# Performance work log

Measured on AMD Instinct MI355X. Metric: run time of the kernel, lower is better.

## Reference

```python
import jax, jax.numpy as jnp
import numpy as np
from jax import lax

B, N, E, H = 512, 128, 256, 8
D = E // H
CLIP = 10.0
NEG = -1e9  # finite stand-in for -inf (backward-safe, math-identical after softmax)


def setup_inputs() -> dict:
    key = jax.random.key(0)
    ks = jax.random.split(key, 5)
    s = lambda k, shape: jax.random.normal(k, shape, jnp.float32) * 0.05
    return {
        "node_embeddings": jax.random.normal(ks[0], (B, N, E), jnp.float32),
        "Wqkv": s(ks[1], (E, 3 * E)), "bqkv": jnp.zeros((3 * E,), jnp.float32),
        "Wfix": s(ks[2], (E, E)), "bfix": jnp.zeros((E,), jnp.float32),
        "Wstep": s(ks[3], (2 * E, E)), "bstep": jnp.zeros((E,), jnp.float32),
        "Wmlp": s(ks[4], (E, E)), "bmlp": jnp.zeros((E,), jnp.float32),
    }


def reference(node_embeddings, Wqkv, bqkv, Wfix, bfix, Wstep, bstep, Wmlp, bmlp):
    scale = 1.0 / np.sqrt(D)
    graph_emb = node_embeddings.mean(axis=1)                       # (B,E)
    qkv = node_embeddings @ Wqkv + bqkv                            # (B,N,3E)
    k, v, logit_k = jnp.split(qkv, 3, axis=-1)
    kh = k.reshape(B, N, H, D).transpose(0, 2, 1, 3)               # (B,H,N,D)
    vh = v.reshape(B, N, H, D).transpose(0, 2, 1, 3)               # (B,H,N,D)
    fixed = graph_emb @ Wfix + bfix                                # (B,E)
    first = node_embeddings[:, 0, :]                               # (B,E)
    bidx = jnp.arange(B)

    def step(carry, _):
        current, visited, logp_sum = carry
        last = node_embeddings[bidx, current]                      # gather last action emb (B,E)
        q = fixed + (jnp.concatenate([first, last], axis=-1) @ Wstep + bstep)
        qh = q.reshape(B, H, D)                                    # single query per head
        attn = jnp.einsum('bhd,bhnd->bhn', qh, kh) * scale
        attn = jnp.where(visited[:, None, :], NEG, attn)
        attn = jax.nn.softmax(attn, axis=-1)
        ctx = jnp.einsum('bhn,bhnd->bhd', attn, vh).reshape(B, E)
        x = ctx @ Wmlp + bmlp                                      # (B,E)
        logits = jnp.einsum('be,bne->bn', x, logit_k) * scale      # (B,N)
        logits = jnp.tanh(logits) * CLIP
        logits = jnp.where(visited, NEG, logits)
        log_p = jax.nn.log_softmax(logits, axis=-1)
        action = jnp.argmax(log_p, axis=-1)                        # greedy decode
        chosen = jnp.take_along_axis(log_p, action[:, None], axis=1)[:, 0]
        visited = visited | jax.nn.one_hot(action, N, dtype=bool)
        return (action, visited, logp_sum + chosen), action

    visited0 = jnp.zeros((B, N), bool).at[:, 0].set(True)
    current0 = jnp.zeros((B,), jnp.int32)
    (_, _, logp_sum), seq = lax.scan(
        step, (current0, visited0, jnp.zeros((B,), jnp.float32)), None, length=N - 1)
    return logp_sum                                                # (B,) summed log-prob of tour
```

## Files before the change

kernel.cpp:

```cpp
#include <hip/hip_runtime.h>
#include <math.h>


#define B_ 512
#define N_ 128
#define E_ 256
#define H_ 8
#define D_ 32
#define NEG (-1.0e9f)
#define CLIPV 10.0f
#define SCALE 0.17677669529663688110f

typedef float v2f __attribute__((ext_vector_type(2)));

__device__ __forceinline__ void pkfma(v2f& acc, v2f a, v2f b) {
  asm("v_pk_fma_f32 %0, %1, %2, %0" : "+v"(acc) : "v"(a), "v"(b));
}

template <int CTRL>
__device__ __forceinline__ float dpp_f(float x) {
  int r = __builtin_amdgcn_update_dpp(__float_as_int(x), __float_as_int(x),
                                      CTRL, 0xf, 0xf, false);
  return __int_as_float(r);
}
template <int CTRL, int RM>
__device__ __forceinline__ float dpp_mv(float x, float idv) {
  int r = __builtin_amdgcn_update_dpp(__float_as_int(idv), __float_as_int(x),
                                      CTRL, RM, 0xf, false);
  return __int_as_float(r);
}
__device__ __forceinline__ float wred_max(float v) {
  v = fmaxf(v, dpp_f<0xB1>(v));
  v = fmaxf(v, dpp_f<0x4E>(v));
  v = fmaxf(v, dpp_f<0x124>(v));
  v = fmaxf(v, dpp_f<0x128>(v));
  v = fmaxf(v, dpp_mv<0x142, 0xa>(v, -1e38f));
  v = fmaxf(v, dpp_mv<0x143, 0xc>(v, -1e38f));
  return __int_as_float(__builtin_amdgcn_readlane(__float_as_int(v), 63));
}
__device__ __forceinline__ float wred_sum(float v) {
  v += dpp_f<0xB1>(v);
  v += dpp_f<0x4E>(v);
  v += dpp_f<0x124>(v);
  v += dpp_f<0x128>(v);
  v += dpp_mv<0x142, 0xa>(v, 0.0f);
  v += dpp_mv<0x143, 0xc>(v, 0.0f);
  return __int_as_float(__builtin_amdgcn_readlane(__float_as_int(v), 63));
}

__global__ void k0_prep(const float* __restrict__ Wqkv, const float* __restrict__ bqkv,
                        const float* __restrict__ Wmlp, const float* __restrict__ bmlp,
                        float* __restrict__ Wc, float* __restrict__ bc,
                        float* __restrict__ wc2, float* __restrict__ cconst) {
  int t = threadIdx.x;
  int blk = blockIdx.x;
  __shared__ float row_s[E_];
  if (blk < E_) {
    int g = blk;
    row_s[t] = Wqkv[g * 768 + 512 + t];
    __syncthreads();
    int f = t;
    const float4* wm4 = (const float4*)(Wmlp + f * E_);
    const float4* w34 = (const float4*)row_s;
    float acc = 0.f;
#pragma unroll 8
    for (int j = 0; j < E_ / 4; ++j) {
      float4 a = w34[j]; float4 bv = wm4[j];
      acc += a.x * bv.x + a.y * bv.y + a.z * bv.z + a.w * bv.w;
    }
    Wc[g * E_ + f] = acc;
  } else {
    int f = t;
    float a1 = 0.f, a2 = 0.f;
    for (int e = 0; e < E_; ++e) {
      a1 += bqkv[512 + e] * Wmlp[f * E_ + e];
      a2 += Wqkv[f * 768 + 512 + e] * bmlp[e];
    }
    bc[f] = a1;
    wc2[f] = a2;
    if (t == 0) {
      float c = 0.f;
      for (int e = 0; e < E_; ++e) c += bqkv[512 + e] * bmlp[e];
      *cconst = c;
    }
  }
}

__global__ __launch_bounds__(256, 2)
void k_gemm(const float* __restrict__ emb, const float* __restrict__ Wqkv,
            const float* __restrict__ bqkv,
            const float* __restrict__ Wc, const float* __restrict__ bc,
            const float* __restrict__ Wstep, const float* __restrict__ qbase,
            float* __restrict__ kk_, float* __restrict__ vv_,
            float* __restrict__ lk2, float* __restrict__ qtab,
            int ncc, int tmask) {
  __shared__ float As[256 * 64];
  int t = threadIdx.x;
  int r0 = blockIdx.x * 64;
  {
    int m = t >> 2;
    int c0 = t & 3;
    const float4* e4 = (const float4*)emb;
#pragma unroll
    for (int p = 0; p < 16; ++p) {
      int c4 = c0 + p * 4;
      float4 a = e4[(size_t)(r0 + m) * 64 + c4];
      As[(c4 * 4 + 0) * 64 + m] = a.x;
      As[(c4 * 4 + 1) * 64 + m] = a.y;
      As[(c4 * 4 + 2) * 64 + m] = a.z;
      As[(c4 * 4 + 3) * 64 + m] = a.w;
    }
  }
  __syncthreads();
  int tx = t & 15, ty = t >> 4;
  const float4* As4 = (const float4*)As;
  for (int cc = 0; cc < ncc; ++cc) {
    const float* Bp; int ldb4; const float* bias; float* outp;
    int colbase = (cc & 1) * 128;
    switch (cc >> 1) {
      case 0:  Bp = Wqkv + colbase;          ldb4 = 192; bias = bqkv + colbase;       outp = kk_; break;
      case 1:  Bp = Wqkv + 256 + colbase;    ldb4 = 192; bias = bqkv + 256 + colbase; outp = vv_; break;
      case 2:  Bp = Wc + colbase;            ldb4 = 64;  bias = bc + colbase;         outp = lk2; break;
      default: Bp = Wstep + 65536 + colbase; ldb4 = 64;
               bias = qbase + (size_t)(r0 >> 7) * 256 + colbase;                      outp = qtab; break;
    }
    const float4* B4 = (const float4*)Bp;
    float acc[4][8];
#pragma unroll
    for (int i = 0; i < 4; ++i)
#pragma unroll
      for (int j = 0; j < 8; ++j) acc[i][j] = 0.f;

#pragma unroll 4
    for (int kk = 0; kk < 256; ++kk) {
      float4 b0 = B4[kk * ldb4 + tx * 2];
      float4 b1 = B4[kk * ldb4 + tx * 2 + 1];
      float4 av = As4[kk * 16 + ty];
      float a_[4] = {av.x, av.y, av.z, av.w};
#pragma unroll
      for (int i = 0; i < 4; ++i) {
        acc[i][0] += a_[i] * b0.x; acc[i][1] += a_[i] * b0.y;
        acc[i][2] += a_[i] * b0.z; acc[i][3] += a_[i] * b0.w;
        acc[i][4] += a_[i] * b1.x; acc[i][5] += a_[i] * b1.y;
        acc[i][6] += a_[i] * b1.z; acc[i][7] += a_[i] * b1.w;
      }
    }
    float bj[8];
#pragma unroll
    for (int j = 0; j < 8; ++j) bj[j] = bias ? bias[tx * 8 + j] : 0.f;
    int tr = (tmask >> (cc >> 1)) & 1;
    if (!tr) {
#pragma unroll
      for (int i = 0; i < 4; ++i) {
        int row = r0 + ty * 4 + i;
        float4 o0 = make_float4(acc[i][0] + bj[0], acc[i][1] + bj[1], acc[i][2] + bj[2], acc[i][3] + bj[3]);
        float4 o1 = make_float4(acc[i][4] + bj[4], acc[i][5] + bj[5], acc[i][6] + bj[6], acc[i][7] + bj[7]);
        float4* o4 = (float4*)(outp + (size_t)row * 256 + colbase + tx * 8);
        o4[0] = o0; o4[1] = o1;
      }
    } else {
#pragma unroll
      for (int i = 0; i < 4; ++i) {
        int row = r0 + ty * 4 + i;
        int bb = row >> 7, nn = row & 127;
        float* op = outp + (size_t)bb * 32768 + nn;
#pragma unroll
        for (int j = 0; j < 8; ++j)
          op[(size_t)(colbase + tx * 8 + j) * 128] = acc[i][j] + bj[j];
      }
    }
  }
}

__global__ void k_qbase(const float* __restrict__ emb, const float* __restrict__ Wfix,
                        const float* __restrict__ bfix, const float* __restrict__ Wstep,
                        const float* __restrict__ bstep, float* __restrict__ qbase) {
  int b = blockIdx.x, t = threadIdx.x;
  __shared__ float ge[E_], fi[E_];
  const float* eb = emb + (size_t)b * N_ * E_;
  float s = 0.f;
#pragma unroll 8
  for (int n = 0; n < N_; ++n) s += eb[n * E_ + t];
  ge[t] = s * (1.0f / 128.0f);
  fi[t] = eb[t];
  __syncthreads();
  float acc = bfix[t] + bstep[t];
#pragma unroll 4
  for (int g = 0; g < E_; ++g)
    acc += ge[g] * Wfix[g * E_ + t] + fi[g] * Wstep[g * E_ + t];
  qbase[b * E_ + t] = acc;
}

__global__ void k_c(const float* __restrict__ emb, const float* __restrict__ wc2,
                    const float* __restrict__ cconst, float* __restrict__ cvec) {
  __shared__ float w[E_];
  int t = threadIdx.x;
  w[t] = wc2[t];
  __syncthreads();
  int row = blockIdx.x * 256 + t;
  const float4* e4 = (const float4*)(emb + (size_t)row * E_);
  const float4* w4 = (const float4*)w;
  float acc = 0.f;
#pragma unroll 8
  for (int j = 0; j < E_ / 4; ++j) {
    float4 a = e4[j], bv = w4[j];
    acc += a.x * bv.x + a.y * bv.y + a.z * bv.z + a.w * bv.w;
  }
  cvec[row] = acc + *cconst;
}

__global__ __attribute__((amdgpu_flat_work_group_size(512, 512), amdgpu_waves_per_eu(2, 2)))
void k_roll(const float* __restrict__ emb, const float* __restrict__ Wstep,
            const float* __restrict__ kT, const float* __restrict__ vv_,
            const float* __restrict__ lkT,
            const float* __restrict__ qbase, const float* __restrict__ cvec,
            const float* __restrict__ qtab, int use_qtab,
            float* __restrict__ out) {
  int lt = threadIdx.x;
  int b = blockIdx.x;
  int h = lt >> 6;
  int j = lt & 63;

  __shared__ float sq_lds[128 * 260];
  __shared__ float work[6144];
  float* at_s  = work;
  float* ctx_s = work + 1024;
  float* zp    = work + 1280;

  if (use_qtab) {
    const float4* qt4 = (const float4*)(qtab + (size_t)b * 32768);
#pragma unroll
    for (int p = 0; p < 16; ++p) {
      int idx = p * 512 + lt;
      int n = idx >> 6, c4 = idx & 63;
      float4 a = qt4[idx];
      *(float4*)(sq_lds + n * 260 + c4 * 4) = a;
    }
  } else {
    float* At = work;
    float* Bs = work + 2048;
    const float4* eb4 = (const float4*)(emb + (size_t)b * 32768);
    const float* W2 = Wstep + 65536;
    int n0 = (lt & 31) * 4;
    int e0 = (lt >> 5) * 16;
    float acc[4][16];
#pragma unroll
    for (int i = 0; i < 4; ++i)
#pragma unroll
      for (int jj = 0; jj < 16; ++jj) acc[i][jj] = 0.f;

    for (int gc = 0; gc < 16; ++gc) {
      {
        int n = lt & 127, q4g = lt >> 7;
        float4 a = eb4[n * 64 + gc * 4 + q4g];
        At[(q4g * 4 + 0) * 128 + n] = a.x;
        At[(q4g * 4 + 1) * 128 + n] = a.y;
        At[(q4g * 4 + 2) * 128 + n] = a.z;
        At[(q4g * 4 + 3) * 128 + n] = a.w;
      }
      {
        const float4* w4 = (const float4*)(W2 + gc * 16 * 256);
        ((float4*)Bs)[lt] = w4[lt];
        ((float4*)Bs)[lt + 512] = w4[lt + 512];
      }
      __syncthreads();
#pragma unroll
      for (int gi = 0; gi < 16; ++gi) {
        float4 a4 = *(const float4*)(At + gi * 128 + n0);
        const float4* bp = (const float4*)(Bs + gi * 256 + e0);
        float4 b0 = bp[0], b1 = bp[1], b2 = bp[2], b3 = bp[3];
        float av[4] = {a4.x, a4.y, a4.z, a4.w};
        float bv[16] = {b0.x, b0.y, b0.z, b0.w, b1.x, b1.y, b1.z, b1.w,
                        b2.x, b2.y, b2.z, b2.w, b3.x, b3.y, b3.z, b3.w};
#pragma unroll
        for (int i = 0; i < 4; ++i)
#pragma unroll
          for (int jj = 0; jj < 16; ++jj) acc[i][jj] += av[i] * bv[jj];
      }
      __syncthreads();
    }
    const float* qb = qbase + (size_t)b * 256;
    float qbr[16];
#pragma unroll
    for (int jj = 0; jj < 16; ++jj) qbr[jj] = qb[e0 + jj];
#pragma unroll
    for (int i = 0; i < 4; ++i)
#pragma unroll
      for (int jj = 0; jj < 16; ++jj)
        sq_lds[(n0 + i) * 260 + e0 + jj] = acc[i][jj] + qbr[jj];
  }
  __syncthreads();
  __builtin_amdgcn_sched_barrier(0);

  const float* kTb = kT + (size_t)b * 32768;
  const float* vb  = vv_ + (size_t)b * 32768;
  const float* lTb = lkT + (size_t)b * 32768;

  v2f k0p[16], k1p[16];
#pragma unroll
  for (int d = 0; d < 16; ++d) {
    k0p[d] = (v2f){kTb[(h * 32 + 2 * d) * 128 + j],      kTb[(h * 32 + 2 * d + 1) * 128 + j]};
    k1p[d] = (v2f){kTb[(h * 32 + 2 * d) * 128 + j + 64], kTb[(h * 32 + 2 * d + 1) * 128 + j + 64]};
    asm("" : "+v"(k0p[d]));
    asm("" : "+v"(k1p[d]));
  }
  int e_own = h * 32 + (j & 31), nh = j >> 5;
  v2f vp[32];
#pragma unroll
  for (int m = 0; m < 32; ++m) {
    vp[m] = (v2f){vb[(nh * 64 + 2 * m) * 256 + e_own], vb[(nh * 64 + 2 * m + 1) * 256 + e_own]};
    asm("" : "+v"(vp[m]));
  }
  v2f l0p[16], l1p[16];
#pragma unroll
  for (int e = 0; e < 16; ++e) {
    l0p[e] = (v2f){lTb[(h * 32 + 2 * e) * 128 + j],      lTb[(h * 32 + 2 * e + 1) * 128 + j]};
    l1p[e] = (v2f){lTb[(h * 32 + 2 * e) * 128 + j + 64], lTb[(h * 32 + 2 * e + 1) * 128 + j + 64]};
    asm("" : "+v"(l0p[e]));
    asm("" : "+v"(l1p[e]));
  }
  float cv_lo = cvec[b * 128 + j];
  float cv_hi = cvec[b * 128 + j + 64];
  int vis_lo = (j == 0) ? 1 : 0, vis_hi = 0;
  int cur = 0;
  float lp = 0.f;
  int rof0 = j * 12;
  int rof1 = rof0 + 768;
  int csw  = h ^ ((j >> 2) & 7);

#pragma unroll 1
  for (int it = 0; it < N_ - 1; ++it) {
    const float4* q4 = (const float4*)(sq_lds + cur * 260 + h * 32);
    v2f s00 = {0.f, 0.f}, s01 = {0.f, 0.f}, s10 = {0.f, 0.f}, s11 = {0.f, 0.f};
#pragma unroll
    for (int dd = 0; dd < 8; ++dd) {
      float4 qv = q4[dd];
      v2f qa = {qv.x, qv.y}, qb = {qv.z, qv.w};
      pkfma(s00, qa, k0p[2 * dd]);
      pkfma(s01, qb, k0p[2 * dd + 1]);
      pkfma(s10, qa, k1p[2 * dd]);
      pkfma(s11, qb, k1p[2 * dd + 1]);
    }
    float slo = vis_lo ? NEG : ((s00.x + s00.y) + (s01.x + s01.y)) * SCALE;
    float shi = vis_hi ? NEG : ((s10.x + s10.y) + (s11.x + s11.y)) * SCALE;
    float m = wred_max(fmaxf(slo, shi));
    float elo = expf(slo - m), ehi = expf(shi - m);
    at_s[h * 128 + j] = elo;
    at_s[h * 128 + 64 + j] = ehi;
    float inv = 1.0f / wred_sum(elo + ehi);
    const float4* a4 = (const float4*)(at_s + h * 128 + nh * 64);
    v2f c0 = {0.f, 0.f}, c1 = {0.f, 0.f};
#pragma unroll
    for (int mm = 0; mm < 16; ++mm) {
      float4 av = a4[mm];
      v2f aa = {av.x, av.y}, ab = {av.z, av.w};
      pkfma(c0, aa, vp[2 * mm]);
      pkfma(c1, ab, vp[2 * mm + 1]);
    }
    float c = (c0.x + c0.y) + (c1.x + c1.y);
    c += __shfl_xor(c, 32);
    c *= inv;
    if (j < 32) ctx_s[h * 32 + j] = c;
    const float4* cx4 = (const float4*)(ctx_s + h * 32);
    v2f z00 = {0.f, 0.f}, z01 = {0.f, 0.f}, z10 = {0.f, 0.f}, z11 = {0.f, 0.f};
#pragma unroll
    for (int ee = 0; ee < 8; ++ee) {
      float4 cv = cx4[ee];
      v2f ca = {cv.x, cv.y}, cb = {cv.z, cv.w};
      pkfma(z00, ca, l0p[2 * ee]);
      pkfma(z01, cb, l0p[2 * ee + 1]);
      pkfma(z10, ca, l1p[2 * ee]);
      pkfma(z11, cb, l1p[2 * ee + 1]);
    }
    float* zpw = zp + (it & 1) * 1536;
    zpw[rof0 + csw] = (z00.x + z00.y) + (z01.x + z01.y);
    zpw[rof1 + csw] = (z10.x + z10.y) + (z11.x + z11.y);
    __syncthreads();

    const float4* zr0 = (const float4*)(zpw + rof0);
    const float4* zr1 = (const float4*)(zpw + rof1);
    float4 za = zr0[0], zb = zr0[1], zc = zr1[0], zd = zr1[1];
    float zlo = cv_lo + ((za.x + za.y) + (za.z + za.w)) + ((zb.x + zb.y) + (zb.z + zb.w));
    float zhi = cv_hi + ((zc.x + zc.y) + (zc.z + zc.w)) + ((zd.x + zd.y) + (zd.z + zd.w));
    float zmlo = vis_lo ? -1e30f : zlo;
    float zmhi = vis_hi ? -1e30f : zhi;
    float vmax = wred_max(fmaxf(zmlo, zmhi));
    unsigned long long blo = __ballot(zmlo == vmax);
    int action;
    if (blo) action = __ffsll((unsigned long long)blo) - 1;
    else     action = 63 + __ffsll((unsigned long long)__ballot(zmhi == vmax));
    if (h == 0) {
      float lmax = CLIPV * tanhf(vmax * SCALE);
      float tlo = vis_lo ? 0.f : expf(CLIPV * tanhf(zlo * SCALE) - 10.0f);
      float thi = vis_hi ? 0.f : expf(CLIPV * tanhf(zhi * SCALE) - 10.0f);
      float S = wred_sum(tlo + thi);
      lp += lmax - 10.0f - logf(S);
    }
    cur = action;
    vis_lo |= (action == j);
    vis_hi |= (action == j + 64);
  }
  if (lt == 0) out[b] = lp;
}

extern "C" void kernel_launch(void* const* d_in, const int* in_sizes, int n_in,
                              void* d_out, int out_size, void* d_ws, size_t ws_size,
                              hipStream_t stream) {
  (void)in_sizes; (void)n_in; (void)out_size;
  const float* emb   = (const float*)d_in[0];
  const float* Wqkv  = (const float*)d_in[1];
  const float* bqkv  = (const float*)d_in[2];
  const float* Wfix  = (const float*)d_in[3];
  const float* bfix  = (const float*)d_in[4];
  const float* Wstep = (const float*)d_in[5];
  const float* bstep = (const float*)d_in[6];
  const float* Wmlp  = (const float*)d_in[7];
  const float* bmlp  = (const float*)d_in[8];
  float* out = (float*)d_out;
  float* ws = (float*)d_ws;

  const size_t NBE = (size_t)B_ * N_ * E_;
  float* kk_    = ws;
  float* vv_    = ws + NBE;
  float* lk2    = ws + 2 * NBE;
  float* qbase  = ws + 3 * NBE;
  float* cvec   = qbase + 131072;
  float* Wc     = cvec + 65536;
  float* bc     = Wc + 65536;
  float* wc2    = bc + 256;
  float* cconst = wc2 + 256;
  size_t qoff   = 3 * NBE + 262720;
  float* qtab   = ws + qoff;
  int use_qtab  = (ws_size >= (qoff + NBE) * sizeof(float)) ? 1 : 0;

  hipLaunchKernelGGL(k0_prep, dim3(257), dim3(256), 0, stream,
                     Wqkv, bqkv, Wmlp, bmlp, Wc, bc, wc2, cconst);
  hipLaunchKernelGGL(k_qbase, dim3(512), dim3(256), 0, stream,
                     emb, Wfix, bfix, Wstep, bstep, qbase);
  hipLaunchKernelGGL(k_c, dim3(256), dim3(256), 0, stream,
                     emb, wc2, cconst, cvec);
  hipLaunchKernelGGL(k_gemm, dim3(1024), dim3(256), 0, stream,
                     emb, Wqkv, bqkv, Wc, bc, Wstep, qbase,
                     kk_, vv_, lk2, qtab, use_qtab ? 8 : 6, 0b0101);
  hipLaunchKernelGGL(k_roll, dim3(512), dim3(512), 0, stream,
                     emb, Wstep, kk_, vv_, lk2, qbase, cvec, qtab, use_qtab, out);
}
```

Before: 1.165 ms.

## Split rollout kernel; read query table from global instead of staging in LDS

Adds a specialized rollout kernel for the precomputed query-table path that drops the 133KB LDS query staging and instead reads the per-step query row straight from global memory using a wave-uniform index. The LDS footprint shrinks to about 17KB and the launch bounds no longer pin waves-per-EU, which could allow more blocks per CU and removes the upfront table copy. The cost is a global/L2 load on the serial per-step critical path, where an LDS read was used before. The fallback kernel keeps the original behaviour.

```diff
diff --git a/kernel.cpp b/kernel.cpp
--- a/kernel.cpp
+++ b/kernel.cpp
@@ -209,88 +209,19 @@
   cvec[row] = acc + *cconst;
 }
 
-__global__ __attribute__((amdgpu_flat_work_group_size(512, 512), amdgpu_waves_per_eu(2, 2)))
-void k_roll(const float* __restrict__ emb, const float* __restrict__ Wstep,
-            const float* __restrict__ kT, const float* __restrict__ vv_,
-            const float* __restrict__ lkT,
-            const float* __restrict__ qbase, const float* __restrict__ cvec,
-            const float* __restrict__ qtab, int use_qtab,
-            float* __restrict__ out) {
+__global__ __launch_bounds__(512)
+void k_rollq(const float* __restrict__ kT, const float* __restrict__ vv_,
+             const float* __restrict__ lkT, const float* __restrict__ cvec,
+             const float* __restrict__ qtab, float* __restrict__ out) {
   int lt = threadIdx.x;
   int b = blockIdx.x;
   int h = lt >> 6;
   int j = lt & 63;
 
-  __shared__ float sq_lds[128 * 260];
-  __shared__ float work[6144];
+  __shared__ float work[4352];
   float* at_s  = work;
   float* ctx_s = work + 1024;
   float* zp    = work + 1280;
-
-  if (use_qtab) {
-    const float4* qt4 = (const float4*)(qtab + (size_t)b * 32768);
-#pragma unroll
-    for (int p = 0; p < 16; ++p) {
-      int idx = p * 512 + lt;
-      int n = idx >> 6, c4 = idx & 63;
-      float4 a = qt4[idx];
-      *(float4*)(sq_lds + n * 260 + c4 * 4) = a;
-    }
-  } else {
-    float* At = work;
-    float* Bs = work + 2048;
-    const float4* eb4 = (const float4*)(emb + (size_t)b * 32768);
-    const float* W2 = Wstep + 65536;
-    int n0 = (lt & 31) * 4;
-    int e0 = (lt >> 5) * 16;
-    float acc[4][16];
-#pragma unroll
-    for (int i = 0; i < 4; ++i)
-#pragma unroll
-      for (int jj = 0; jj < 16; ++jj) acc[i][jj] = 0.f;
-
-    for (int gc = 0; gc < 16; ++gc) {
-      {
-        int n = lt & 127, q4g = lt >> 7;
-        float4 a = eb4[n * 64 + gc * 4 + q4g];
-        At[(q4g * 4 + 0) * 128 + n] = a.x;
-        At[(q4g * 4 + 1) * 128 + n] = a.y;
-        At[(q4g * 4 + 2) * 128 + n] = a.z;
-        At[(q4g * 4 + 3) * 128 + n] = a.w;
-      }
-      {
-        const float4* w4 = (const float4*)(W2 + gc * 16 * 256);
-        ((float4*)Bs)[lt] = w4[lt];
-        ((float4*)Bs)[lt + 512] = w4[lt + 512];
-      }
-      __syncthreads();
-#pragma unroll
-      for (int gi = 0; gi < 16; ++gi) {
-        float4 a4 = *(const float4*)(At + gi * 128 + n0);
-        const float4* bp = (const float4*)(Bs + gi * 256 + e0);
-        float4 b0 = bp[0], b1 = bp[1], b2 = bp[2], b3 = bp[3];
-        float av[4] = {a4.x, a4.y, a4.z, a4.w};
-        float bv[16] = {b0.x, b0.y, b0.z, b0.w, b1.x, b1.y, b1.z, b1.w,
-                        b2.x, b2.y, b2.z, b2.w, b3.x, b3.y, b3.z, b3.w};
-#pragma unroll
-        for (int i = 0; i < 4; ++i)
-#pragma unroll
-          for (int jj = 0; jj < 16; ++jj) acc[i][jj] += av[i] * bv[jj];
-      }
-      __syncthreads();
-    }
-    const float* qb = qbase + (size_t)b * 256;
-    float qbr[16];
-#pragma unroll
-    for (int jj = 0; jj < 16; ++jj) qbr[jj] = qb[e0 + jj];
-#pragma unroll
-    for (int i = 0; i < 4; ++i)
-#pragma unroll
-      for (int jj = 0; jj < 16; ++jj)
-        sq_lds[(n0 + i) * 260 + e0 + jj] = acc[i][jj] + qbr[jj];
-  }
-  __syncthreads();
-  __builtin_amdgcn_sched_barrier(0);
 
   const float* kTb = kT + (size_t)b * 32768;
   const float* vb  = vv_ + (size_t)b * 32768;
@@ -327,10 +258,12 @@
   int rof0 = j * 12;
   int rof1 = rof0 + 768;
   int csw  = h ^ ((j >> 2) & 7);
+  const float* qhb = qtab + ((size_t)b << 15) + (h << 5);
 
 #pragma unroll 1
   for (int it = 0; it < N_ - 1; ++it) {
-    const float4* q4 = (const float4*)(sq_lds + cur * 260 + h * 32);
+    int curu = __builtin_amdgcn_readfirstlane(cur);
+    const float4* q4 = (const float4*)(qhb + (curu << 8));
     v2f s00 = {0.f, 0.f}, s01 = {0.f, 0.f}, s10 = {0.f, 0.f}, s11 = {0.f, 0.f};
 #pragma unroll
     for (int dd = 0; dd < 8; ++dd) {
@@ -403,6 +336,190 @@
   if (lt == 0) out[b] = lp;
 }
 
+__global__ __attribute__((amdgpu_flat_work_group_size(512, 512), amdgpu_waves_per_eu(2, 2)))
+void k_roll(const float* __restrict__ emb, const float* __restrict__ Wstep,
+            const float* __restrict__ kT, const float* __restrict__ vv_,
+            const float* __restrict__ lkT,
+            const float* __restrict__ qbase, const float* __restrict__ cvec,
+            float* __restrict__ out) {
+  int lt = threadIdx.x;
+  int b = blockIdx.x;
+  int h = lt >> 6;
+  int j = lt & 63;
+
+  __shared__ float sq_lds[128 * 260];
+  __shared__ float work[6144];
+  float* at_s  = work;
+  float* ctx_s = work + 1024;
+  float* zp    = work + 1280;
+
+  {
+    float* At = work;
+    float* Bs = work + 2048;
+    const float4* eb4 = (const float4*)(emb + (size_t)b * 32768);
+    const float* W2 = Wstep + 65536;
+    int n0 = (lt & 31) * 4;
+    int e0 = (lt >> 5) * 16;
+    float acc[4][16];
+#pragma unroll
+    for (int i = 0; i < 4; ++i)
+#pragma unroll
+      for (int jj = 0; jj < 16; ++jj) acc[i][jj] = 0.f;
+
+    for (int gc = 0; gc < 16; ++gc) {
+      {
+        int n = lt & 127, q4g = lt >> 7;
+        float4 a = eb4[n * 64 + gc * 4 + q4g];
+        At[(q4g * 4 + 0) * 128 + n] = a.x;
+        At[(q4g * 4 + 1) * 128 + n] = a.y;
+        At[(q4g * 4 + 2) * 128 + n] = a.z;
+        At[(q4g * 4 + 3) * 128 + n] = a.w;
+      }
+      {
+        const float4* w4 = (const float4*)(W2 + gc * 16 * 256);
+        ((float4*)Bs)[lt] = w4[lt];
+        ((float4*)Bs)[lt + 512] = w4[lt + 512];
+      }
+      __syncthreads();
+#pragma unroll
+      for (int gi = 0; gi < 16; ++gi) {
+        float4 a4 = *(const float4*)(At + gi * 128 + n0);
+        const float4* bp = (const float4*)(Bs + gi * 256 + e0);
+        float4 b0 = bp[0], b1 = bp[1], b2 = bp[2], b3 = bp[3];
+        float av[4] = {a4.x, a4.y, a4.z, a4.w};
+        float bv[16] = {b0.x, b0.y, b0.z, b0.w, b1.x, b1.y, b1.z, b1.w,
+                        b2.x, b2.y, b2.z, b2.w, b3.x, b3.y, b3.z, b3.w};
+#pragma unroll
+        for (int i = 0; i < 4; ++i)
+#pragma unroll
+          for (int jj = 0; jj < 16; ++jj) acc[i][jj] += av[i] * bv[jj];
+      }
+      __syncthreads();
+    }
+    const float* qb = qbase + (size_t)b * 256;
+    float qbr[16];
+#pragma unroll
+    for (int jj = 0; jj < 16; ++jj) qbr[jj] = qb[e0 + jj];
+#pragma unroll
+    for (int i = 0; i < 4; ++i)
+#pragma unroll
+      for (int jj = 0; jj < 16; ++jj)
+        sq_lds[(n0 + i) * 260 + e0 + jj] = acc[i][jj] + qbr[jj];
+  }
+  __syncthreads();
+  __builtin_amdgcn_sched_barrier(0);
+
+  const float* kTb = kT + (size_t)b * 32768;
+  const float* vb  = vv_ + (size_t)b * 32768;
+  const float* lTb = lkT + (size_t)b * 32768;
+
+  v2f k0p[16], k1p[16];
+#pragma unroll
+  for (int d = 0; d < 16; ++d) {
+    k0p[d] = (v2f){kTb[(h * 32 + 2 * d) * 128 + j],      kTb[(h * 32 + 2 * d + 1) * 128 + j]};
+    k1p[d] = (v2f){kTb[(h * 32 + 2 * d) * 128 + j + 64], kTb[(h * 32 + 2 * d + 1) * 128 + j + 64]};
+    asm("" : "+v"(k0p[d]));
+    asm("" : "+v"(k1p[d]));
+  }
+  int e_own = h * 32 + (j & 31), nh = j >> 5;
+  v2f vp[32];
+#pragma unroll
+  for (int m = 0; m < 32; ++m) {
+    vp[m] = (v2f){vb[(nh * 64 + 2 * m) * 256 + e_own], vb[(nh * 64 + 2 * m + 1) * 256 + e_own]};
+    asm("" : "+v"(vp[m]));
+  }
+  v2f l0p[16], l1p[16];
+#pragma unroll
+  for (int e = 0; e < 16; ++e) {
+    l0p[e] = (v2f){lTb[(h * 32 + 2 * e) * 128 + j],      lTb[(h * 32 + 2 * e + 1) * 128 + j]};
+    l1p[e] = (v2f){lTb[(h * 32 + 2 * e) * 128 + j + 64], lTb[(h * 32 + 2 * e + 1) * 128 + j + 64]};
+    asm("" : "+v"(l0p[e]));
+    asm("" : "+v"(l1p[e]));
+  }
+  float cv_lo = cvec[b * 128 + j];
+  float cv_hi = cvec[b * 128 + j + 64];
+  int vis_lo = (j == 0) ? 1 : 0, vis_hi = 0;
+  int cur = 0;
+  float lp = 0.f;
+  int rof0 = j * 12;
+  int rof1 = rof0 + 768;
+  int csw  = h ^ ((j >> 2) & 7);
+
+#pragma unroll 1
+  for (int it = 0; it < N_ - 1; ++it) {
+    const float4* q4 = (const float4*)(sq_lds + cur * 260 + h * 32);
+    v2f s00 = {0.f, 0.f}, s01 = {0.f, 0.f}, s10 = {0.f, 0.f}, s11 = {0.f, 0.f};
+#pragma unroll
+    for (int dd = 0; dd < 8; ++dd) {
+      float4 qv = q4[dd];
+      v2f qa = {qv.x, qv.y}, qb = {qv.z, qv.w};
+      pkfma(s00, qa, k0p[2 * dd]);
+      pkfma(s01, qb, k0p[2 * dd + 1]);
+      pkfma(s10, qa, k1p[2 * dd]);
+      pkfma(s11, qb, k1p[2 * dd + 1]);
+    }
+    float slo = vis_lo ? NEG : ((s00.x + s00.y) + (s01.x + s01.y)) * SCALE;
+    float shi = vis_hi ? NEG : ((s10.x + s10.y) + (s11.x + s11.y)) * SCALE;
+    float m = wred_max(fmaxf(slo, shi));
+    float elo = expf(slo - m), ehi = expf(shi - m);
+    at_s[h * 128 + j] = elo;
+    at_s[h * 128 + 64 + j] = ehi;
+    float inv = 1.0f / wred_sum(elo + ehi);
+    const float4* a4 = (const float4*)(at_s + h * 128 + nh * 64);
+    v2f c0 = {0.f, 0.f}, c1 = {0.f, 0.f};
+#pragma unroll
+    for (int mm = 0; mm < 16; ++mm) {
+      float4 av = a4[mm];
+      v2f aa = {av.x, av.y}, ab = {av.z, av.w};
+      pkfma(c0, aa, vp[2 * mm]);
+      pkfma(c1, ab, vp[2 * mm + 1]);
+    }
+    float c = (c0.x + c0.y) + (c1.x + c1.y);
+    c += __shfl_xor(c, 32);
+    c *= inv;
+    if (j < 32) ctx_s[h * 32 + j] = c;
+    const float4* cx4 = (const float4*)(ctx_s + h * 32);
+    v2f z00 = {0.f, 0.f}, z01 = {0.f, 0.f}, z10 = {0.f, 0.f}, z11 = {0.f, 0.f};
+#pragma unroll
+    for (int ee = 0; ee < 8; ++ee) {
+      float4 cv = cx4[ee];
+      v2f ca = {cv.x, cv.y}, cb = {cv.z, cv.w};
+      pkfma(z00, ca, l0p[2 * ee]);
+      pkfma(z01, cb, l0p[2 * ee + 1]);
+      pkfma(z10, ca, l1p[2 * ee]);
+      pkfma(z11, cb, l1p[2 * ee + 1]);
+    }
+    float* zpw = zp + (it & 1) * 1536;
+    zpw[rof0 + csw] = (z00.x + z00.y) + (z01.x + z01.y);
+    zpw[rof1 + csw] = (z10.x + z10.y) + (z11.x + z11.y);
+    __syncthreads();
+
+    const float4* zr0 = (const float4*)(zpw + rof0);
+    const float4* zr1 = (const float4*)(zpw + rof1);
+    float4 za = zr0[0], zb = zr0[1], zc = zr1[0], zd = zr1[1];
+    float zlo = cv_lo + ((za.x + za.y) + (za.z + za.w)) + ((zb.x + zb.y) + (zb.z + zb.w));
+    float zhi = cv_hi + ((zc.x + zc.y) + (zc.z + zc.w)) + ((zd.x + zd.y) + (zd.z + zd.w));
+    float zmlo = vis_lo ? -1e30f : zlo;
+    float zmhi = vis_hi ? -1e30f : zhi;
+    float vmax = wred_max(fmaxf(zmlo, zmhi));
+    unsigned long long blo = __ballot(zmlo == vmax);
+    int action;
+    if (blo) action = __ffsll((unsigned long long)blo) - 1;
+    else     action = 63 + __ffsll((unsigned long long)__ballot(zmhi == vmax));
+    if (h == 0) {
+      float lmax = CLIPV * tanhf(vmax * SCALE);
+      float tlo = vis_lo ? 0.f : expf(CLIPV * tanhf(zlo * SCALE) - 10.0f);
+      float thi = vis_hi ? 0.f : expf(CLIPV * tanhf(zhi * SCALE) - 10.0f);
+      float S = wred_sum(tlo + thi);
+      lp += lmax - 10.0f - logf(S);
+    }
+    cur = action;
+    vis_lo |= (action == j);
+    vis_hi |= (action == j + 64);
+  }
+  if (lt == 0) out[b] = lp;
+}
+
 extern "C" void kernel_launch(void* const* d_in, const int* in_sizes, int n_in,
                               void* d_out, int out_size, void* d_ws, size_t ws_size,
                               hipStream_t stream) {
@@ -442,6 +559,11 @@
   hipLaunchKernelGGL(k_gemm, dim3(1024), dim3(256), 0, stream,
                      emb, Wqkv, bqkv, Wc, bc, Wstep, qbase,
                      kk_, vv_, lk2, qtab, use_qtab ? 8 : 6, 0b0101);
-  hipLaunchKernelGGL(k_roll, dim3(512), dim3(512), 0, stream,
-                     emb, Wstep, kk_, vv_, lk2, qbase, cvec, qtab, use_qtab, out);
-}
+  if (use_qtab) {
+    hipLaunchKernelGGL(k_rollq, dim3(512), dim3(512), 0, stream,
+                       kk_, vv_, lk2, cvec, qtab, out);
+  } else {
+    hipLaunchKernelGGL(k_roll, dim3(512), dim3(512), 0, stream,
+                       emb, Wstep, kk_, vv_, lk2, qbase, cvec, out);
+  }
+}
```

Result: no change. 1.176 ms (+1.0%).

## Move per-node query table to a global buffer and read it from memory per step

Applied to the files above, without the earlier changes.

The precomputed query table now always lives in a static device-global buffer filled by the GEMM kernel, so the fallback in-kernel GEMM path and workspace-size check are gone. The rollout kernel no longer stages the 128x256 table in LDS and instead loads the current node's query row directly from global memory each step using a uniform address. This cuts LDS use (about 133 KB down to about 17 KB per block), which should allow more blocks per CU and removes the upfront staging copy. In exchange, each step's query load goes to global memory (L2) instead of LDS, which lengthens the serial dependency chain.

```diff
diff --git a/kernel.cpp b/kernel.cpp
--- a/kernel.cpp
+++ b/kernel.cpp
@@ -10,6 +10,8 @@
 #define NEG (-1.0e9f)
 #define CLIPV 10.0f
 #define SCALE 0.17677669529663688110f
+
+__device__ float g_qtab[(size_t)B_ * N_ * E_];
 
 typedef float v2f __attribute__((ext_vector_type(2)));
 
@@ -92,8 +94,7 @@
             const float* __restrict__ Wc, const float* __restrict__ bc,
             const float* __restrict__ Wstep, const float* __restrict__ qbase,
             float* __restrict__ kk_, float* __restrict__ vv_,
-            float* __restrict__ lk2, float* __restrict__ qtab,
-            int ncc, int tmask) {
+            float* __restrict__ lk2, int ncc, int tmask) {
   __shared__ float As[256 * 64];
   int t = threadIdx.x;
   int r0 = blockIdx.x * 64;
@@ -122,7 +123,7 @@
       case 1:  Bp = Wqkv + 256 + colbase;    ldb4 = 192; bias = bqkv + 256 + colbase; outp = vv_; break;
       case 2:  Bp = Wc + colbase;            ldb4 = 64;  bias = bc + colbase;         outp = lk2; break;
       default: Bp = Wstep + 65536 + colbase; ldb4 = 64;
-               bias = qbase + (size_t)(r0 >> 7) * 256 + colbase;                      outp = qtab; break;
+               bias = qbase + (size_t)(r0 >> 7) * 256 + colbase;                      outp = g_qtab; break;
     }
     const float4* B4 = (const float4*)Bp;
     float acc[4][8];
@@ -209,88 +210,19 @@
   cvec[row] = acc + *cconst;
 }
 
-__global__ __attribute__((amdgpu_flat_work_group_size(512, 512), amdgpu_waves_per_eu(2, 2)))
-void k_roll(const float* __restrict__ emb, const float* __restrict__ Wstep,
-            const float* __restrict__ kT, const float* __restrict__ vv_,
-            const float* __restrict__ lkT,
-            const float* __restrict__ qbase, const float* __restrict__ cvec,
-            const float* __restrict__ qtab, int use_qtab,
-            float* __restrict__ out) {
+__global__ __launch_bounds__(512)
+void k_rollq(const float* __restrict__ kT, const float* __restrict__ vv_,
+             const float* __restrict__ lkT, const float* __restrict__ cvec,
+             float* __restrict__ out) {
   int lt = threadIdx.x;
   int b = blockIdx.x;
   int h = lt >> 6;
   int j = lt & 63;
 
-  __shared__ float sq_lds[128 * 260];
-  __shared__ float work[6144];
+  __shared__ float work[4352];
   float* at_s  = work;
   float* ctx_s = work + 1024;
   float* zp    = work + 1280;
-
-  if (use_qtab) {
-    const float4* qt4 = (const float4*)(qtab + (size_t)b * 32768);
-#pragma unroll
-    for (int p = 0; p < 16; ++p) {
-      int idx = p * 512 + lt;
-      int n = idx >> 6, c4 = idx & 63;
-      float4 a = qt4[idx];
-      *(float4*)(sq_lds + n * 260 + c4 * 4) = a;
-    }
-  } else {
-    float* At = work;
-    float* Bs = work + 2048;
-    const float4* eb4 = (const float4*)(emb + (size_t)b * 32768);
-    const float* W2 = Wstep + 65536;
-    int n0 = (lt & 31) * 4;
-    int e0 = (lt >> 5) * 16;
-    float acc[4][16];
-#pragma unroll
-    for (int i = 0; i < 4; ++i)
-#pragma unroll
-      for (int jj = 0; jj < 16; ++jj) acc[i][jj] = 0.f;
-
-    for (int gc = 0; gc < 16; ++gc) {
-      {
-        int n = lt & 127, q4g = lt >> 7;
-        float4 a = eb4[n * 64 + gc * 4 + q4g];
-        At[(q4g * 4 + 0) * 128 + n] = a.x;
-        At[(q4g * 4 + 1) * 128 + n] = a.y;
-        At[(q4g * 4 + 2) * 128 + n] = a.z;
-        At[(q4g * 4 + 3) * 128 + n] = a.w;
-      }
-      {
-        const float4* w4 = (const float4*)(W2 + gc * 16 * 256);
-        ((float4*)Bs)[lt] = w4[lt];
-        ((float4*)Bs)[lt + 512] = w4[lt + 512];
-      }
-      __syncthreads();
-#pragma unroll
-      for (int gi = 0; gi < 16; ++gi) {
-        float4 a4 = *(const float4*)(At + gi * 128 + n0);
-        const float4* bp = (const float4*)(Bs + gi * 256 + e0);
-        float4 b0 = bp[0], b1 = bp[1], b2 = bp[2], b3 = bp[3];
-        float av[4] = {a4.x, a4.y, a4.z, a4.w};
-        float bv[16] = {b0.x, b0.y, b0.z, b0.w, b1.x, b1.y, b1.z, b1.w,
-                        b2.x, b2.y, b2.z, b2.w, b3.x, b3.y, b3.z, b3.w};
-#pragma unroll
-        for (int i = 0; i < 4; ++i)
-#pragma unroll
-          for (int jj = 0; jj < 16; ++jj) acc[i][jj] += av[i] * bv[jj];
-      }
-      __syncthreads();
-    }
-    const float* qb = qbase + (size_t)b * 256;
-    float qbr[16];
-#pragma unroll
-    for (int jj = 0; jj < 16; ++jj) qbr[jj] = qb[e0 + jj];
-#pragma unroll
-    for (int i = 0; i < 4; ++i)
-#pragma unroll
-      for (int jj = 0; jj < 16; ++jj)
-        sq_lds[(n0 + i) * 260 + e0 + jj] = acc[i][jj] + qbr[jj];
-  }
-  __syncthreads();
-  __builtin_amdgcn_sched_barrier(0);
 
   const float* kTb = kT + (size_t)b * 32768;
   const float* vb  = vv_ + (size_t)b * 32768;
@@ -327,10 +259,12 @@
   int rof0 = j * 12;
   int rof1 = rof0 + 768;
   int csw  = h ^ ((j >> 2) & 7);
+  const float* qhb = g_qtab + ((size_t)b << 15) + (h << 5);
 
 #pragma unroll 1
   for (int it = 0; it < N_ - 1; ++it) {
-    const float4* q4 = (const float4*)(sq_lds + cur * 260 + h * 32);
+    int curu = __builtin_amdgcn_readfirstlane(cur);
+    const float4* q4 = (const float4*)(qhb + (curu << 8));
     v2f s00 = {0.f, 0.f}, s01 = {0.f, 0.f}, s10 = {0.f, 0.f}, s11 = {0.f, 0.f};
 #pragma unroll
     for (int dd = 0; dd < 8; ++dd) {
@@ -406,7 +340,7 @@
 extern "C" void kernel_launch(void* const* d_in, const int* in_sizes, int n_in,
                               void* d_out, int out_size, void* d_ws, size_t ws_size,
                               hipStream_t stream) {
-  (void)in_sizes; (void)n_in; (void)out_size;
+  (void)in_sizes; (void)n_in; (void)out_size; (void)ws_size;
   const float* emb   = (const float*)d_in[0];
   const float* Wqkv  = (const float*)d_in[1];
   const float* bqkv  = (const float*)d_in[2];
@@ -429,9 +363,6 @@
   float* bc     = Wc + 65536;
   float* wc2    = bc + 256;
   float* cconst = wc2 + 256;
-  size_t qoff   = 3 * NBE + 262720;
-  float* qtab   = ws + qoff;
-  int use_qtab  = (ws_size >= (qoff + NBE) * sizeof(float)) ? 1 : 0;
 
   hipLaunchKernelGGL(k0_prep, dim3(257), dim3(256), 0, stream,
                      Wqkv, bqkv, Wmlp, bmlp, Wc, bc, wc2, cconst);
@@ -441,7 +372,7 @@
                      emb, wc2, cconst, cvec);
   hipLaunchKernelGGL(k_gemm, dim3(1024), dim3(256), 0, stream,
                      emb, Wqkv, bqkv, Wc, bc, Wstep, qbase,
-                     kk_, vv_, lk2, qtab, use_qtab ? 8 : 6, 0b0101);
-  hipLaunchKernelGGL(k_roll, dim3(512), dim3(512), 0, stream,
-                     emb, Wstep, kk_, vv_, lk2, qbase, cvec, qtab, use_qtab, out);
-}
+                     kk_, vv_, lk2, 8, 0b0101);
+  hipLaunchKernelGGL(k_rollq, dim3(512), dim3(512), 0, stream,
+                     kk_, vv_, lk2, cvec, out);
+}
```

Result: slower. 1.460 ms (+25.3%).
